# Kernel tuning notes

Hardware: AMD Instinct MI355X
Metric: run time of the kernel (lower is better)

Reference implementation:

```python
import jax, jax.numpy as jnp
import numpy as np

C = 64       # channels; must equal W due to the module's final-Linear-over-W quirk
D = 768      # context_dim (CLIP)
G = 32       # GroupNorm groups
EPS = 1e-5


def setup_inputs() -> dict:
    key = jax.random.key(0)
    ks = jax.random.split(key, 10)
    s = 0.02
    return {
        "x": jax.random.normal(ks[0], (4, C, 64, 64), jnp.float32),
        "context": jax.random.normal(ks[1], (4, 77, D), jnp.float32),
        "gn_scale": jnp.ones((C,), jnp.float32),
        "gn_bias": jnp.zeros((C,), jnp.float32),
        "qkv_w": jax.random.normal(ks[2], (3 * C, C), jnp.float32) * s,  # conv1x1 (out,in)
        "qkv_b": jnp.zeros((3 * C,), jnp.float32),
        "proj_w": jax.random.normal(ks[3], (C, C), jnp.float32) * s,
        "proj_b": jnp.zeros((C,), jnp.float32),
        "ln_scale": jnp.ones((C,), jnp.float32),
        "ln_bias": jnp.zeros((C,), jnp.float32),
        "wq": jax.random.normal(ks[4], (C, C), jnp.float32) * s,   # stored (in,out)
        "bq": jnp.zeros((C,), jnp.float32),
        "wk": jax.random.normal(ks[5], (D, C), jnp.float32) * s,
        "bk": jnp.zeros((C,), jnp.float32),
        "wv": jax.random.normal(ks[6], (D, C), jnp.float32) * s,
        "bv": jnp.zeros((C,), jnp.float32),
        "wo": jax.random.normal(ks[7], (C, C), jnp.float32) * s,
        "bo": jnp.zeros((C,), jnp.float32),
    }


def _group_norm(x, scale, bias):
    B, Ch, H, W = x.shape
    xg = x.reshape(B, G, Ch // G, H, W)
    mu = xg.mean(axis=(2, 3, 4), keepdims=True)
    var = xg.var(axis=(2, 3, 4), keepdims=True)
    xn = ((xg - mu) * jax.lax.rsqrt(var + EPS)).reshape(B, Ch, H, W)
    return xn * scale[None, :, None, None] + bias[None, :, None, None]


def _layer_norm(x, scale, bias):
    mu = x.mean(-1, keepdims=True)
    var = x.var(-1, keepdims=True)
    return (x - mu) * jax.lax.rsqrt(var + EPS) * scale + bias


def reference(x, context, gn_scale, gn_bias, qkv_w, qkv_b, proj_w, proj_b,
              ln_scale, ln_bias, wq, bq, wk, bk, wv, bv, wo, bo):
    B, Ch, H, W = x.shape
    N = H * W
    scale = 1.0 / jnp.sqrt(jnp.asarray(Ch, x.dtype))

    # --- self-attention over spatial positions ---
    h = _group_norm(x, gn_scale, gn_bias)
    qkv = jnp.einsum('bchw,oc->bhwo', h, qkv_w) + qkv_b     # conv 1x1 -> (B,H,W,3C)
    qkv = qkv.reshape(B, N, 3 * Ch)
    q, k, v = jnp.split(qkv, 3, axis=-1)                    # each (B,N,C)
    attn = jax.nn.softmax(jnp.einsum('bnc,bmc->bnm', q, k) * scale, axis=-1)
    self_out = jnp.einsum('bnm,bmc->bnc', attn, v)
    self_out = self_out.transpose(0, 2, 1).reshape(B, Ch, H, W)
    h = x + jnp.einsum('bchw,oc->bohw', self_out, proj_w) + proj_b[None, :, None, None]

    # --- cross-attention with text context ---
    tf = _layer_norm(h.reshape(B, Ch, N).transpose(0, 2, 1), ln_scale, ln_bias)  # (B,N,C)
    tq = tf @ wq + bq                                        # (B,N,C)
    tk = context @ wk + bk                                   # (B,T,C)
    tv = context @ wv + bv                                   # (B,T,C)
    tattn = jax.nn.softmax(jnp.einsum('bnc,btc->bnt', tq, tk) * scale, axis=-1)
    tout = jnp.einsum('bnt,btc->bnc', tattn, tv)             # (B,N,C)
    t4 = tout.transpose(0, 2, 1).reshape(B, Ch, H, W)
    # faithful to source: extra transpose(1,2)+reshape scramble, then Linear over last axis (W==C)
    scr = jnp.transpose(t4, (0, 2, 1, 3)).reshape(B, Ch, H, W)
    h = h + scr @ wo + bo
    return h
```

## Files before the change

kernel.cpp:

```cpp
#include <hip/hip_runtime.h>
#include <cstdint>
#include <cstddef>

#define BN 4
#define CN 64
#define NN 4096
#define GN 32
#define TN 77
#define DN 768
#define EPSV 1e-5f
#define SCALEV 0.125f
#define LOG2E 1.4426950408889634f
#define NSPLIT 8

typedef __bf16 bf16_t;
typedef __attribute__((ext_vector_type(8))) __bf16 bf16x8;
typedef __attribute__((ext_vector_type(4))) __bf16 bf16x4;
typedef __attribute__((ext_vector_type(4))) float f32x4;

#define EXP2(x) __builtin_amdgcn_exp2f(x)

__device__ __forceinline__ f32x4 mfma16(bf16x8 a, bf16x8 b, f32x4 c) {
  return __builtin_amdgcn_mfma_f32_16x16x32_bf16(a, b, c, 0, 0, 0);
}
__device__ __forceinline__ f32x4 zero4() { return (f32x4){0.f, 0.f, 0.f, 0.f}; }

__device__ __forceinline__ void gload16(const void* g, void* l) {
  __builtin_amdgcn_global_load_lds(
      (const __attribute__((address_space(1))) void*)g,
      (__attribute__((address_space(3))) void*)l, 16, 0, 0);
}

__device__ __forceinline__ int fragpos(int o) {
  return ((o >> 2) & 3) * 16 + ((o >> 4) & 1) * 4 + ((o >> 5) & 1) * 8 + (o & 3);
}
__device__ __forceinline__ int vperm(int p) {
  return (p & 32) + ((p >> 2) & 3) * 8 + ((p >> 4) & 1) * 4 + (p & 3);
}
__device__ __forceinline__ int perm96(int t) {
  int u = t & 31;
  return (t & ~31) + (((u & 15) >> 2) << 3) + ((u >> 4) << 2) + (u & 3);
}

__global__ __launch_bounds__(256) void k_pre(const float* __restrict__ x,
    float* __restrict__ gpart,
    const float* __restrict__ ctx,
    const float* __restrict__ wk, const float* __restrict__ bk,
    const float* __restrict__ wv, const float* __restrict__ bv,
    bf16_t* __restrict__ tko, bf16_t* __restrict__ tvo) {
  __shared__ float ss[4], ssq[4];
  __shared__ float cr[768];
  __shared__ float red[4][64];
  int bx = blockIdx.x;
  int tid = threadIdx.x;
  if (bx < 256) {
    const float4* base = reinterpret_cast<const float4*>(x + (size_t)bx * 4096);
    float s = 0.f, sq = 0.f;
    for (int i = tid; i < 1024; i += 256) {
      float4 v = base[i];
      s  += v.x + v.y + v.z + v.w;
      sq += v.x*v.x + v.y*v.y + v.z*v.z + v.w*v.w;
    }
    for (int off = 32; off; off >>= 1) { s += __shfl_down(s, off); sq += __shfl_down(sq, off); }
    int w = tid >> 6, l = tid & 63;
    if (l == 0) { ss[w] = s; ssq[w] = sq; }
    __syncthreads();
    if (tid == 0) {
      gpart[bx * 2]     = ss[0] + ss[1] + ss[2] + ss[3];
      gpart[bx * 2 + 1] = ssq[0] + ssq[1] + ssq[2] + ssq[3];
    }
    return;
  }
  int bt = bx - 256;
  int b = bt / 96, t = bt % 96;
  if (t >= 77) {
    if (tid < 64) {
      if (t < 80) tko[((size_t)(b * 80) + t) * 64 + tid] = (bf16_t)0.f;
      tvo[((size_t)(b * 64) + tid) * 96 + perm96(t)] = (bf16_t)0.f;
    }
    return;
  }
  const float* src = ctx + ((size_t)(b * TN) + t) * 768;
  for (int i = tid; i < 768; i += 256) cr[i] = src[i];
  __syncthreads();
  int o = tid & 63, sec = tid >> 6;
  int sel = sec & 1, dh = sec >> 1;
  const float* w = (sel ? wv : wk) + dh * 384 * 64;
  const float* c0 = cr + dh * 384;
  float acc = 0.f;
  for (int d = 0; d < 384; d++) acc += c0[d] * w[d * 64 + o];
  red[sec][o] = acc;
  __syncthreads();
  if (tid < 128) {
    int s2 = tid >> 6; int oo = tid & 63;
    float r = red[s2][oo] + red[s2 + 2][oo] + (s2 ? bv[oo] : bk[oo]);
    if (s2 == 0)
      tko[((size_t)(b * 80) + t) * 64 + (fragpos(oo) ^ ((t & 7) << 3))] = (bf16_t)r;
    else
      tvo[((size_t)(b * 64) + oo) * 96 + perm96(t)] = (bf16_t)r;
  }
}

__global__ __launch_bounds__(256) void k_gn_qkv(const float* __restrict__ x,
    const float* __restrict__ gpart,
    const float* __restrict__ gns, const float* __restrict__ gnb,
    const float* __restrict__ qkvw, const float* __restrict__ qkvb,
    bf16_t* __restrict__ qb, bf16_t* __restrict__ kb, bf16_t* __restrict__ vT) {
  __shared__ float hn[64][36];
  __shared__ float wqkT[64][129];
  __shared__ float wv2[64][64];
  int bx = blockIdx.x; int b = bx >> 7; int t0 = (bx & 127) << 5;
  int tid = threadIdx.x;
  for (int i = tid; i < 2048; i += 256) {
    float4 v = reinterpret_cast<const float4*>(qkvw)[i];
    int base = i << 2; int o = base >> 6, cc = base & 63;
    wqkT[cc][o] = v.x; wqkT[cc + 1][o] = v.y; wqkT[cc + 2][o] = v.z; wqkT[cc + 3][o] = v.w;
  }
  for (int i = tid; i < 1024; i += 256) {
    float4 v = reinterpret_cast<const float4*>(qkvw + 8192)[i];
    int base = i << 2; int ch = base >> 6, cc = base & 63;
    *reinterpret_cast<float4*>(&wv2[ch][cc]) = v;
  }
  {
    int c = tid >> 2, p0 = (tid & 3) << 3;
    float4 gp = *reinterpret_cast<const float4*>(gpart + (((b << 5) + (c >> 1)) << 2));
    float mu = (gp.x + gp.z) * (1.f / 8192.f);
    float e2 = (gp.y + gp.w) * (1.f / 8192.f);
    float rs = rsqrtf(e2 - mu * mu + EPSV);
    float sc = gns[c] * rs, bi = gnb[c] - mu * sc;
    const float* xp = x + ((size_t)(b * 64 + c)) * NN + t0 + p0;
    float4 v1 = *reinterpret_cast<const float4*>(xp);
    float4 v2 = *reinterpret_cast<const float4*>(xp + 4);
    hn[c][p0+0] = v1.x*sc+bi; hn[c][p0+1] = v1.y*sc+bi;
    hn[c][p0+2] = v1.z*sc+bi; hn[c][p0+3] = v1.w*sc+bi;
    hn[c][p0+4] = v2.x*sc+bi; hn[c][p0+5] = v2.y*sc+bi;
    hn[c][p0+6] = v2.z*sc+bi; hn[c][p0+7] = v2.w*sc+bi;
  }
  __syncthreads();
  {
    int o0 = tid & 63, p0 = (tid >> 6) << 3;
    int pq = fragpos(o0);
    float acc0[8], acc1[8];
    float b0 = qkvb[o0], b1 = qkvb[64 + o0];
    #pragma unroll
    for (int m = 0; m < 8; m++) { acc0[m] = b0; acc1[m] = b1; }
    for (int cc = 0; cc < 64; ++cc) {
      float4 h0 = *reinterpret_cast<const float4*>(&hn[cc][p0]);
      float4 h1 = *reinterpret_cast<const float4*>(&hn[cc][p0 + 4]);
      float w0 = wqkT[cc][o0];
      float w1 = wqkT[cc][64 + o0];
      acc0[0] += h0.x*w0; acc0[1] += h0.y*w0; acc0[2] += h0.z*w0; acc0[3] += h0.w*w0;
      acc0[4] += h1.x*w0; acc0[5] += h1.y*w0; acc0[6] += h1.z*w0; acc0[7] += h1.w*w0;
      acc1[0] += h0.x*w1; acc1[1] += h0.y*w1; acc1[2] += h0.z*w1; acc1[3] += h0.w*w1;
      acc1[4] += h1.x*w1; acc1[5] += h1.y*w1; acc1[6] += h1.z*w1; acc1[7] += h1.w*w1;
    }
    size_t rowbase = ((size_t)(b * NN) + t0 + p0) << 6;
    #pragma unroll
    for (int j = 0; j < 8; j++) {
      qb[rowbase + ((size_t)j << 6) + pq] = (bf16_t)(acc0[j] * (SCALEV * LOG2E));
      kb[rowbase + ((size_t)j << 6) + (pq ^ (j << 3))] = (bf16_t)acc1[j];
    }
  }
  {
    int p2 = tid & 31, ob = tid >> 5;
    int kk = t0 + p2;
    int colsw = vperm(kk & 63) ^ (ob << 3);
    float acc[8];
    #pragma unroll
    for (int m = 0; m < 8; m++) acc[m] = qkvb[128 + ob + 8*m];
    for (int c0 = 0; c0 < 64; c0 += 4) {
      float h0 = hn[c0][p2], h1 = hn[c0+1][p2], h2 = hn[c0+2][p2], h3 = hn[c0+3][p2];
      #pragma unroll
      for (int m = 0; m < 8; m++) {
        float4 w4 = *reinterpret_cast<const float4*>(&wv2[ob + 8*m][c0]);
        acc[m] += h0*w4.x + h1*w4.y + h2*w4.z + h3*w4.w;
      }
    }
    size_t vbase = ((size_t)(b * 64)) * NN + (size_t)(kk & ~63) + colsw;
    #pragma unroll
    for (int m = 0; m < 8; m++)
      vT[vbase + (size_t)(ob + 8*m) * NN] = (bf16_t)acc[m];
  }
}

__global__ __launch_bounds__(256, 4) void k_attn(const bf16_t* __restrict__ qb,
    const bf16_t* __restrict__ kb, const bf16_t* __restrict__ vT,
    bf16_t* __restrict__ opart, float* __restrict__ mpart, float* __restrict__ lpart) {
  __shared__ __align__(16) bf16_t smem[2][8192];
  int bx = blockIdx.x;
  int xcd = bx & 7;
  int b = xcd >> 1;
  int inner = ((bx >> 3) << 1) | (xcd & 1);
  int split = inner >> 5;
  int qblk = inner & 31;
  int tid = threadIdx.x; int w = tid >> 6, l = tid & 63;
  int lo = l & 15, g = l >> 4;
  int qbase = (qblk << 7) + (w << 5);
  const bf16_t* qrowA = qb + (((size_t)(b * NN) + qbase + lo) << 6) + g * 16;
  const bf16_t* qrowB = qrowA + (16 << 6);
  bf16x8 qfA0 = *reinterpret_cast<const bf16x8*>(qrowA);
  bf16x8 qfA1 = *reinterpret_cast<const bf16x8*>(qrowA + 8);
  bf16x8 qfB0 = *reinterpret_cast<const bf16x8*>(qrowB);
  bf16x8 qfB1 = *reinterpret_cast<const bf16x8*>(qrowB + 8);
  f32x4 oaccA[4], oaccB[4];
  #pragma unroll
  for (int nt = 0; nt < 4; nt++) {
    oaccA[nt] = zero4();
    oaccB[nt] = zero4();
  }
  float mA = -8.f, lA = 0.f, mB = -8.f, lB = 0.f;
  const bf16_t* kbB = kb + ((size_t)b * NN << 6);
  const bf16_t* vB  = vT + ((size_t)b * 64) * NN;
  int kt0 = split << 9;

  int off0 = tid * 8;
  int off1 = 2048 + tid * 8;
  int ch0 = off0 >> 6, sl0 = off0 & 63;
  int ch1 = off1 >> 6, sl1 = off1 & 63;

  {
    const bf16_t* kT = kbB + ((size_t)kt0 << 6);
    gload16(kT + off0, &smem[0][off0]);
    gload16(kT + off1, &smem[0][off1]);
    gload16(vB + (size_t)ch0 * NN + kt0 + sl0, &smem[0][4096 + off0]);
    gload16(vB + (size_t)ch1 * NN + kt0 + sl1, &smem[0][4096 + off1]);
  }
  __syncthreads();

  #pragma unroll 1
  for (int t = 0; t < 8; ++t) {
    int cur = t & 1;
    if (t < 7) {
      int kn = kt0 + ((t + 1) << 6);
      const bf16_t* kT = kbB + ((size_t)kn << 6);
      gload16(kT + off0, &smem[cur ^ 1][off0]);
      gload16(kT + off1, &smem[cur ^ 1][off1]);
      gload16(vB + (size_t)ch0 * NN + kn + sl0, &smem[cur ^ 1][4096 + off0]);
      gload16(vB + (size_t)ch1 * NN + kn + sl1, &smem[cur ^ 1][4096 + off1]);
    }
    const bf16_t* sK = smem[cur];
    const bf16_t* sV = smem[cur] + 4096;
    f32x4 sA[4], sB[4];
    #pragma unroll
    for (int c = 0; c < 4; c++) {
      int kk = (c << 4) + lo;
      int o1 = (g << 4) ^ ((kk & 7) << 3);
      bf16x8 kf0 = *reinterpret_cast<const bf16x8*>(sK + (kk << 6) + o1);
      bf16x8 kf1 = *reinterpret_cast<const bf16x8*>(sK + (kk << 6) + (o1 ^ 8));
      sA[c] = mfma16(kf0, qfA0, zero4());
      sA[c] = mfma16(kf1, qfA1, sA[c]);
      sB[c] = mfma16(kf0, qfB0, zero4());
      sB[c] = mfma16(kf1, qfB1, sB[c]);
    }
    float pmaxA = -1e30f, pmaxB = -1e30f;
    #pragma unroll
    for (int c = 0; c < 4; c++)
      #pragma unroll
      for (int r = 0; r < 4; r++) {
        pmaxA = fmaxf(pmaxA, sA[c][r]);
        pmaxB = fmaxf(pmaxB, sB[c][r]);
      }
    if (!__all(pmaxA - mA <= 8.f)) {
      pmaxA = fmaxf(pmaxA, __shfl_xor(pmaxA, 16));
      pmaxA = fmaxf(pmaxA, __shfl_xor(pmaxA, 32));
      float mn = fmaxf(mA, pmaxA);
      float corr = EXP2(mA - mn);
      lA *= corr; mA = mn;
      float fr[4];
      #pragma unroll
      for (int r = 0; r < 4; r++) fr[r] = __shfl(corr, (g << 2) + r);
      #pragma unroll
      for (int nt = 0; nt < 4; nt++)
        #pragma unroll
        for (int r = 0; r < 4; r++) oaccA[nt][r] *= fr[r];
    }
    if (!__all(pmaxB - mB <= 8.f)) {
      pmaxB = fmaxf(pmaxB, __shfl_xor(pmaxB, 16));
      pmaxB = fmaxf(pmaxB, __shfl_xor(pmaxB, 32));
      float mn = fmaxf(mB, pmaxB);
      float corr = EXP2(mB - mn);
      lB *= corr; mB = mn;
      float fr[4];
      #pragma unroll
      for (int r = 0; r < 4; r++) fr[r] = __shfl(corr, (g << 2) + r);
      #pragma unroll
      for (int nt = 0; nt < 4; nt++)
        #pragma unroll
        for (int r = 0; r < 4; r++) oaccB[nt][r] *= fr[r];
    }
    bf16x8 vf[4];
    #pragma unroll
    for (int nt = 0; nt < 4; nt++) {
      int ch = lo + (nt << 4);
      vf[nt] = *reinterpret_cast<const bf16x8*>(sV + (ch << 6) + ((g ^ (ch & 7)) << 3));
    }
    float lsA0 = 0.f, lsA1 = 0.f, lsB0 = 0.f, lsB1 = 0.f;
    #pragma unroll
    for (int c = 0; c < 4; c++)
      #pragma unroll
      for (int r = 0; r < 4; r++) {
        float pa = EXP2(sA[c][r] - mA);
        float pb = EXP2(sB[c][r] - mB);
        sA[c][r] = pa; sB[c][r] = pb;
        if (c & 1) { lsA1 += pa; lsB1 += pb; } else { lsA0 += pa; lsB0 += pb; }
      }
    lA += lsA0 + lsA1;
    lB += lsB0 + lsB1;
    bf16x8 paA0, paA1, paB0, paB1;
    #pragma unroll
    for (int i = 0; i < 8; i++) {
      paA0[i] = (bf16_t)sA[i >> 2][i & 3]; paA1[i] = (bf16_t)sA[2 + (i >> 2)][i & 3];
      paB0[i] = (bf16_t)sB[i >> 2][i & 3]; paB1[i] = (bf16_t)sB[2 + (i >> 2)][i & 3];
    }
    #pragma unroll
    for (int nt = 0; nt < 4; ++nt) {
      oaccA[nt] = mfma16(paA0, vf[nt], oaccA[nt]);
      oaccB[nt] = mfma16(paB0, vf[nt], oaccB[nt]);
    }
    #pragma unroll
    for (int nt = 0; nt < 4; nt++) {
      int ch = lo + (nt << 4);
      vf[nt] = *reinterpret_cast<const bf16x8*>(sV + (ch << 6) + (((4 + g) ^ (ch & 7)) << 3));
    }
    #pragma unroll
    for (int nt = 0; nt < 4; ++nt) {
      oaccA[nt] = mfma16(paA1, vf[nt], oaccA[nt]);
      oaccB[nt] = mfma16(paB1, vf[nt], oaccB[nt]);
    }
    __syncthreads();
  }

  lA += __shfl_xor(lA, 16); lA += __shfl_xor(lA, 32);
  lB += __shfl_xor(lB, 16); lB += __shfl_xor(lB, 32);

  size_t ob = ((size_t)(split * BN + b)) * NN + qbase;
  float liA[4], liB[4];
  #pragma unroll
  for (int r = 0; r < 4; r++) {
    liA[r] = 1.0f / __shfl(lA, (g << 2) + r);
    liB[r] = 1.0f / __shfl(lB, (g << 2) + r);
  }
  #pragma unroll
  for (int nt = 0; nt < 4; nt++)
    #pragma unroll
    for (int r = 0; r < 4; r++) {
      opart[((ob + (g << 2) + r) << 6) + lo + (nt << 4)] = (bf16_t)(oaccA[nt][r] * liA[r]);
      opart[((ob + 16 + (g << 2) + r) << 6) + lo + (nt << 4)] = (bf16_t)(oaccB[nt][r] * liB[r]);
    }
  if (l < 16) { mpart[ob + l] = mA; lpart[ob + l] = lA; }
  else if (l < 32) { mpart[ob + 16 + lo] = mB; lpart[ob + 16 + lo] = lB; }
}

__global__ __launch_bounds__(256) void k_proj_ln_tq(const float* __restrict__ x,
    const bf16_t* __restrict__ opart, const float* __restrict__ mpart, const float* __restrict__ lpart,
    const float* __restrict__ projw, const float* __restrict__ projb,
    const float* __restrict__ lns, const float* __restrict__ lnb,
    const float* __restrict__ wq, const float* __restrict__ bq,
    float* __restrict__ h2, bf16_t* __restrict__ tq) {
  __shared__ float wcomb[16][NSPLIT];
  __shared__ float sob[16][65];
  __shared__ float h2l[64][17];
  __shared__ float r1[16][16], r2[16][16];
  __shared__ float mu_s[16], rs_s[16];
  int bx = blockIdx.x; int b = bx >> 8; int t0 = (bx & 255) << 4;
  int tid = threadIdx.x;
  if (tid < 16) {
    int p = tid, q = t0 + p;
    float ms[NSPLIT];
    float mstar = -1e30f;
    #pragma unroll
    for (int s = 0; s < NSPLIT; s++) {
      ms[s] = mpart[((size_t)(s * BN + b)) * NN + q];
      mstar = fmaxf(mstar, ms[s]);
    }
    float co[NSPLIT]; float denom = 0.f;
    #pragma unroll
    for (int s = 0; s < NSPLIT; s++) {
      co[s] = EXP2(ms[s] - mstar) * lpart[((size_t)(s * BN + b)) * NN + q];
      denom += co[s];
    }
    float inv = 1.0f / denom;
    #pragma unroll
    for (int s = 0; s < NSPLIT; s++) wcomb[p][s] = co[s] * inv;
  }
  __syncthreads();
  {
    int p = tid >> 4, c0 = (tid & 15) << 2;
    int q = t0 + p;
    float acc[4] = {0.f, 0.f, 0.f, 0.f};
    #pragma unroll
    for (int s = 0; s < NSPLIT; s++) {
      bf16x4 v = *reinterpret_cast<const bf16x4*>(
          opart + ((((size_t)(s * BN + b)) * NN + q) << 6) + c0);
      float wv = wcomb[p][s];
      #pragma unroll
      for (int j = 0; j < 4; j++) acc[j] += wv * (float)v[j];
    }
    #pragma unroll
    for (int j = 0; j < 4; j++) sob[p][c0 + j] = acc[j];
  }
  __syncthreads();
  {
    int p = tid & 15, ob = tid >> 4;
    float acc[4];
    #pragma unroll
    for (int m = 0; m < 4; m++) {
      int o = ob + 16*m;
      acc[m] = projb[o] + x[((size_t)(b * 64) + o) * NN + t0 + p];
    }
    for (int cc = 0; cc < 64; ++cc) {
      float sv = sob[p][cc];
      #pragma unroll
      for (int m = 0; m < 4; m++) acc[m] += sv * projw[(ob + 16*m) * 64 + cc];
    }
    #pragma unroll
    for (int m = 0; m < 4; m++) {
      int o = ob + 16*m;
      h2[((size_t)(b * 64) + o) * NN + t0 + p] = acc[m];
      h2l[o][p] = acc[m];
    }
  }
  __syncthreads();
  {
    int p = tid & 15, og = tid >> 4;
    float s = 0.f, sq = 0.f;
    #pragma unroll
    for (int j = 0; j < 4; j++) { float v = h2l[og * 4 + j][p]; s += v; sq += v*v; }
    r1[og][p] = s; r2[og][p] = sq;
  }
  __syncthreads();
  if (tid < 16) {
    float s = 0.f, sq = 0.f;
    #pragma unroll
    for (int j = 0; j < 16; j++) { s += r1[j][tid]; sq += r2[j][tid]; }
    float mu = s * (1.f/64.f);
    float var = sq * (1.f/64.f) - mu*mu;
    mu_s[tid] = mu; rs_s[tid] = rsqrtf(var + EPSV);
  }
  __syncthreads();
  {
    int p = tid & 15, cb = tid >> 4;
    float mu = mu_s[p], rs = rs_s[p];
    #pragma unroll
    for (int m = 0; m < 4; m++) {
      int c = cb + 16*m;
      sob[p][c] = (h2l[c][p] - mu) * rs * lns[c] + lnb[c];
    }
  }
  __syncthreads();
  {
    int o = tid & 63, pb = tid >> 6;
    int pq = fragpos(o);
    float acc[4];
    #pragma unroll
    for (int m = 0; m < 4; m++) acc[m] = bq[o];
    for (int cc = 0; cc < 64; ++cc) {
      float wv = wq[cc * 64 + o];
      #pragma unroll
      for (int m = 0; m < 4; m++) acc[m] += sob[pb + 4*m][cc] * wv;
    }
    #pragma unroll
    for (int m = 0; m < 4; m++) {
      int p = pb + 4*m;
      tq[(((size_t)(b * NN) + t0 + p) << 6) + pq] = (bf16_t)(acc[m] * (SCALEV * LOG2E));
    }
  }
}

__global__ __launch_bounds__(256) void k_crossf(const bf16_t* __restrict__ tq,
    const bf16_t* __restrict__ tk, const bf16_t* __restrict__ tv,
    const float* __restrict__ wo, const float* __restrict__ bo,
    const float* __restrict__ h2, float* __restrict__ out) {
  __shared__ __align__(16) bf16_t tkl[80][64];
  __shared__ __align__(16) bf16_t tvl[64][104];
  __shared__ __align__(16) bf16_t woT[64][64];
  __shared__ __align__(16) bf16_t toutT[64][64];
  int bx = blockIdx.x; int b = bx >> 6; int c1 = bx & 63;
  int tid = threadIdx.x; int wv_ = tid >> 6; int l = tid & 63;
  int lo = l & 15, g = l >> 4;
  {
    const uint4* src = reinterpret_cast<const uint4*>(tk + (size_t)b * 80 * 64);
    uint4* dst = reinterpret_cast<uint4*>(&tkl[0][0]);
    for (int i = tid; i < 640; i += 256) dst[i] = src[i];
  }
  {
    const uint4* src = reinterpret_cast<const uint4*>(tv + (size_t)b * 64 * 96);
    uint4* dst = reinterpret_cast<uint4*>(&tvl[0][0]);
    for (int i = tid; i < 768; i += 256) {
      int row = i / 12, j = i % 12;
      dst[row * 13 + j] = src[i];
    }
  }
  for (int i = tid; i < 4096; i += 256) {
    int k = i >> 6, w = i & 63;
    int vp = vperm(k);
    woT[w][(((vp >> 3) ^ (w & 7)) << 3) + (vp & 7)] = (bf16_t)wo[i];
  }
  __syncthreads();
  int n0 = (c1 << 6) + (wv_ << 4);
  const bf16_t* qrow = tq + (((size_t)(b * NN) + n0 + lo) << 6) + g * 16;
  bf16x8 qf0 = *reinterpret_cast<const bf16x8*>(qrow);
  bf16x8 qf1 = *reinterpret_cast<const bf16x8*>(qrow + 8);
  f32x4 sa[5];
  #pragma unroll
  for (int ti = 0; ti < 5; ti++) {
    int tok = ti * 16 + lo;
    int o1 = (g << 4) ^ ((tok & 7) << 3);
    bf16x8 kf0 = *reinterpret_cast<const bf16x8*>(&tkl[tok][0] + o1);
    bf16x8 kf1 = *reinterpret_cast<const bf16x8*>(&tkl[tok][0] + (o1 ^ 8));
    f32x4 z = mfma16(kf0, qf0, zero4());
    sa[ti] = mfma16(kf1, qf1, z);
  }
  float p[5][4];
  float mx = -1e30f;
  #pragma unroll
  for (int ti = 0; ti < 5; ti++)
    #pragma unroll
    for (int r = 0; r < 4; r++)
      if (ti * 16 + (g << 2) + r < TN) mx = fmaxf(mx, sa[ti][r]);
  mx = fmaxf(mx, __shfl_xor(mx, 16));
  mx = fmaxf(mx, __shfl_xor(mx, 32));
  float ls = 0.f;
  #pragma unroll
  for (int ti = 0; ti < 5; ti++)
    #pragma unroll
    for (int r = 0; r < 4; r++) {
      float pv = (ti * 16 + (g << 2) + r < TN) ? EXP2(sa[ti][r] - mx) : 0.f;
      p[ti][r] = pv; ls += pv;
    }
  ls += __shfl_xor(ls, 16); ls += __shfl_xor(ls, 32);
  float linv = 1.0f / ls;
  bf16x8 pa[3];
  #pragma unroll
  for (int c = 0; c < 3; c++)
    #pragma unroll
    for (int i = 0; i < 8; i++)
      pa[c][i] = (bf16_t)p[2 * c + (i >> 2)][i & 3];
  f32x4 oacc[4];
  #pragma unroll
  for (int nt = 0; nt < 4; nt++) oacc[nt] = zero4();
  #pragma unroll
  for (int c = 0; c < 3; c++)
    #pragma unroll
    for (int nt = 0; nt < 4; nt++) {
      bf16x8 vf = *reinterpret_cast<const bf16x8*>(&tvl[nt * 16 + lo][0] + c * 32 + g * 8);
      oacc[nt] = mfma16(pa[c], vf, oacc[nt]);
    }
  float li[4];
  #pragma unroll
  for (int r = 0; r < 4; r++) li[r] = __shfl(linv, (g << 2) + r);
  int hh = wv_ & 1, cp = wv_ >> 1;
  #pragma unroll
  for (int nt = 0; nt < 4; nt++) {
    int ch = nt * 16 + lo;
    int basegroup = cp * 4 + g;
    int col = ((basegroup ^ (ch & 7)) << 3) + hh * 4;
    bf16_t tmp[4];
    #pragma unroll
    for (int r = 0; r < 4; r++) tmp[r] = (bf16_t)(oacc[nt][r] * li[r]);
    *reinterpret_cast<uint2*>(&toutT[ch][col]) = *reinterpret_cast<const uint2*>(tmp);
  }
  __syncthreads();
  f32x4 o2[4];
  #pragma unroll
  for (int wt = 0; wt < 4; wt++) o2[wt] = zero4();
  #pragma unroll
  for (int f = 0; f < 2; f++) {
    int c2r = wv_ * 16 + lo;
    int agrp = ((f * 4 + g) ^ (c2r & 7)) << 3;
    bf16x8 af = *reinterpret_cast<const bf16x8*>(&toutT[c2r][agrp]);
    #pragma unroll
    for (int wt = 0; wt < 4; wt++) {
      int wrow = wt * 16 + lo;
      int bgrp = ((f * 4 + g) ^ (wrow & 7)) << 3;
      bf16x8 bf_ = *reinterpret_cast<const bf16x8*>(&woT[wrow][bgrp]);
      o2[wt] = mfma16(af, bf_, o2[wt]);
    }
  }
  const float* h2r = h2 + ((size_t)(b * 64) + c1) * NN;
  float* outr = out + ((size_t)(b * 64) + c1) * NN;
  float bov[4];
  #pragma unroll
  for (int wt = 0; wt < 4; wt++) bov[wt] = bo[wt * 16 + lo];
  #pragma unroll
  for (int wt = 0; wt < 4; wt++)
    #pragma unroll
    for (int r = 0; r < 4; r++) {
      int c2 = wv_ * 16 + (g << 2) + r;
      int pos = (c2 << 6) + wt * 16 + lo;
      outr[pos] = o2[wt][r] + h2r[pos] + bov[wt];
    }
}

extern "C" void kernel_launch(void* const* d_in, const int* in_sizes, int n_in,
                              void* d_out, int out_size, void* d_ws, size_t ws_size,
                              hipStream_t stream) {
  const float* x     = (const float*)d_in[0];
  const float* ctx   = (const float*)d_in[1];
  const float* gns   = (const float*)d_in[2];
  const float* gnb   = (const float*)d_in[3];
  const float* qkvw  = (const float*)d_in[4];
  const float* qkvb  = (const float*)d_in[5];
  const float* projw = (const float*)d_in[6];
  const float* projb = (const float*)d_in[7];
  const float* lns   = (const float*)d_in[8];
  const float* lnb   = (const float*)d_in[9];
  const float* wq    = (const float*)d_in[10];
  const float* bq    = (const float*)d_in[11];
  const float* wk    = (const float*)d_in[12];
  const float* bk    = (const float*)d_in[13];
  const float* wv    = (const float*)d_in[14];
  const float* bv    = (const float*)d_in[15];
  const float* wo    = (const float*)d_in[16];
  const float* bo    = (const float*)d_in[17];
  float* out = (float*)d_out;

  char* ws = (char*)d_ws;
  float* gpart = (float*)ws;
  bf16_t* qb   = (bf16_t*)(ws + 4096);
  bf16_t* kbuf = qb + (size_t)BN * NN * 64;
  bf16_t* vT   = kbuf + (size_t)BN * NN * 64;
  bf16_t* opart = vT + (size_t)BN * NN * 64;
  float* mpart = (float*)(opart + (size_t)NSPLIT * BN * NN * 64);
  float* lpart = mpart + (size_t)NSPLIT * BN * NN;
  float* h2    = lpart + (size_t)NSPLIT * BN * NN;
  bf16_t* tkb16 = (bf16_t*)(h2 + (size_t)BN * NN * 64);
  bf16_t* tvb16 = tkb16 + (size_t)BN * 80 * 64;
  bf16_t* tqb16 = qb;

  k_pre<<<dim3(256 + BN * 96), dim3(256), 0, stream>>>(x, gpart, ctx, wk, bk, wv, bv,
                                                       tkb16, tvb16);
  k_gn_qkv<<<dim3(512), dim3(256), 0, stream>>>(x, gpart, gns, gnb, qkvw, qkvb,
                                                qb, kbuf, vT);
  k_attn<<<dim3(1024), dim3(256), 0, stream>>>(qb, kbuf, vT, opart, mpart, lpart);
  k_proj_ln_tq<<<dim3(1024), dim3(256), 0, stream>>>(x, opart, mpart, lpart, projw, projb,
                                                     lns, lnb, wq, bq, h2, tqb16);
  k_crossf<<<dim3(256), dim3(256), 0, stream>>>(tqb16, tkb16, tvb16, wo, bo, h2, out);
}
```

Before: 76.22 us.

## Process 64 query rows per wave in self-attention to double K/V reuse

Each wave in the attention kernel now handles four 16-row query fragments instead of two. This halves the number of blocks and doubles how much work each K/V tile staged in shared memory feeds into the MFMAs, cutting LDS and global traffic per query. The lazy-rescale skip based on a wave vote is dropped, so the max correction now always runs. Register pressure rises, the occupancy hint is relaxed, and with fewer blocks latency hiding may be weaker.

```diff
diff --git a/kernel.cpp b/kernel.cpp
--- a/kernel.cpp
+++ b/kernel.cpp
@@ -183,7 +183,7 @@
   }
 }
 
-__global__ __launch_bounds__(256, 4) void k_attn(const bf16_t* __restrict__ qb,
+__global__ __launch_bounds__(256) void k_attn(const bf16_t* __restrict__ qb,
     const bf16_t* __restrict__ kb, const bf16_t* __restrict__ vT,
     bf16_t* __restrict__ opart, float* __restrict__ mpart, float* __restrict__ lpart) {
   __shared__ __align__(16) bf16_t smem[2][8192];
@@ -191,24 +191,25 @@
   int xcd = bx & 7;
   int b = xcd >> 1;
   int inner = ((bx >> 3) << 1) | (xcd & 1);
-  int split = inner >> 5;
-  int qblk = inner & 31;
+  int split = inner >> 4;
+  int qblk = inner & 15;
   int tid = threadIdx.x; int w = tid >> 6, l = tid & 63;
   int lo = l & 15, g = l >> 4;
-  int qbase = (qblk << 7) + (w << 5);
-  const bf16_t* qrowA = qb + (((size_t)(b * NN) + qbase + lo) << 6) + g * 16;
-  const bf16_t* qrowB = qrowA + (16 << 6);
-  bf16x8 qfA0 = *reinterpret_cast<const bf16x8*>(qrowA);
-  bf16x8 qfA1 = *reinterpret_cast<const bf16x8*>(qrowA + 8);
-  bf16x8 qfB0 = *reinterpret_cast<const bf16x8*>(qrowB);
-  bf16x8 qfB1 = *reinterpret_cast<const bf16x8*>(qrowB + 8);
-  f32x4 oaccA[4], oaccB[4];
-  #pragma unroll
-  for (int nt = 0; nt < 4; nt++) {
-    oaccA[nt] = zero4();
-    oaccB[nt] = zero4();
-  }
-  float mA = -8.f, lA = 0.f, mB = -8.f, lB = 0.f;
+  int qbase = (qblk << 8) + (w << 6);
+  bf16x8 qf[4][2];
+  #pragma unroll
+  for (int F = 0; F < 4; F++) {
+    const bf16_t* qrow = qb + (((size_t)(b * NN) + qbase + F * 16 + lo) << 6) + g * 16;
+    qf[F][0] = *reinterpret_cast<const bf16x8*>(qrow);
+    qf[F][1] = *reinterpret_cast<const bf16x8*>(qrow + 8);
+  }
+  f32x4 oacc[4][4];
+  #pragma unroll
+  for (int F = 0; F < 4; F++)
+    #pragma unroll
+    for (int nt = 0; nt < 4; nt++) oacc[F][nt] = zero4();
+  float m_[4] = {-8.f, -8.f, -8.f, -8.f};
+  float l_[4] = {0.f, 0.f, 0.f, 0.f};
   const bf16_t* kbB = kb + ((size_t)b * NN << 6);
   const bf16_t* vB  = vT + ((size_t)b * 64) * NN;
   int kt0 = split << 9;
@@ -240,53 +241,38 @@
     }
     const bf16_t* sK = smem[cur];
     const bf16_t* sV = smem[cur] + 4096;
-    f32x4 sA[4], sB[4];
+    f32x4 s[4][4];
     #pragma unroll
     for (int c = 0; c < 4; c++) {
       int kk = (c << 4) + lo;
       int o1 = (g << 4) ^ ((kk & 7) << 3);
       bf16x8 kf0 = *reinterpret_cast<const bf16x8*>(sK + (kk << 6) + o1);
       bf16x8 kf1 = *reinterpret_cast<const bf16x8*>(sK + (kk << 6) + (o1 ^ 8));
-      sA[c] = mfma16(kf0, qfA0, zero4());
-      sA[c] = mfma16(kf1, qfA1, sA[c]);
-      sB[c] = mfma16(kf0, qfB0, zero4());
-      sB[c] = mfma16(kf1, qfB1, sB[c]);
-    }
-    float pmaxA = -1e30f, pmaxB = -1e30f;
-    #pragma unroll
-    for (int c = 0; c < 4; c++)
-      #pragma unroll
-      for (int r = 0; r < 4; r++) {
-        pmaxA = fmaxf(pmaxA, sA[c][r]);
-        pmaxB = fmaxf(pmaxB, sB[c][r]);
+      #pragma unroll
+      for (int F = 0; F < 4; F++) {
+        s[F][c] = mfma16(kf0, qf[F][0], zero4());
+        s[F][c] = mfma16(kf1, qf[F][1], s[F][c]);
       }
-    if (!__all(pmaxA - mA <= 8.f)) {
-      pmaxA = fmaxf(pmaxA, __shfl_xor(pmaxA, 16));
-      pmaxA = fmaxf(pmaxA, __shfl_xor(pmaxA, 32));
-      float mn = fmaxf(mA, pmaxA);
-      float corr = EXP2(mA - mn);
-      lA *= corr; mA = mn;
+    }
+    #pragma unroll
+    for (int F = 0; F < 4; F++) {
+      float pmax = -1e30f;
+      #pragma unroll
+      for (int c = 0; c < 4; c++)
+        #pragma unroll
+        for (int r = 0; r < 4; r++) pmax = fmaxf(pmax, s[F][c][r]);
+      pmax = fmaxf(pmax, __shfl_xor(pmax, 16));
+      pmax = fmaxf(pmax, __shfl_xor(pmax, 32));
+      float mn = fmaxf(m_[F], pmax);
+      float corr = EXP2(m_[F] - mn);
+      l_[F] *= corr; m_[F] = mn;
       float fr[4];
       #pragma unroll
       for (int r = 0; r < 4; r++) fr[r] = __shfl(corr, (g << 2) + r);
       #pragma unroll
       for (int nt = 0; nt < 4; nt++)
         #pragma unroll
-        for (int r = 0; r < 4; r++) oaccA[nt][r] *= fr[r];
-    }
-    if (!__all(pmaxB - mB <= 8.f)) {
-      pmaxB = fmaxf(pmaxB, __shfl_xor(pmaxB, 16));
-      pmaxB = fmaxf(pmaxB, __shfl_xor(pmaxB, 32));
-      float mn = fmaxf(mB, pmaxB);
-      float corr = EXP2(mB - mn);
-      lB *= corr; mB = mn;
-      float fr[4];
-      #pragma unroll
-      for (int r = 0; r < 4; r++) fr[r] = __shfl(corr, (g << 2) + r);
-      #pragma unroll
-      for (int nt = 0; nt < 4; nt++)
-        #pragma unroll
-        for (int r = 0; r < 4; r++) oaccB[nt][r] *= fr[r];
+        for (int r = 0; r < 4; r++) oacc[F][nt][r] *= fr[r];
     }
     bf16x8 vf[4];
     #pragma unroll
@@ -294,61 +280,68 @@
       int ch = lo + (nt << 4);
       vf[nt] = *reinterpret_cast<const bf16x8*>(sV + (ch << 6) + ((g ^ (ch & 7)) << 3));
     }
-    float lsA0 = 0.f, lsA1 = 0.f, lsB0 = 0.f, lsB1 = 0.f;
-    #pragma unroll
-    for (int c = 0; c < 4; c++)
-      #pragma unroll
-      for (int r = 0; r < 4; r++) {
-        float pa = EXP2(sA[c][r] - mA);
-        float pb = EXP2(sB[c][r] - mB);
-        sA[c][r] = pa; sB[c][r] = pb;
-        if (c & 1) { lsA1 += pa; lsB1 += pb; } else { lsA0 += pa; lsB0 += pb; }
+    #pragma unroll
+    for (int F = 0; F < 4; F++) {
+      float ls0 = 0.f, ls1 = 0.f;
+      #pragma unroll
+      for (int c = 0; c < 4; c++)
+        #pragma unroll
+        for (int r = 0; r < 4; r++) {
+          float pv = EXP2(s[F][c][r] - m_[F]);
+          s[F][c][r] = pv;
+          if (c & 1) ls1 += pv; else ls0 += pv;
+        }
+      l_[F] += ls0 + ls1;
+    }
+    bf16x8 pa[4][2];
+    #pragma unroll
+    for (int F = 0; F < 4; F++)
+      #pragma unroll
+      for (int i = 0; i < 8; i++) {
+        pa[F][0][i] = (bf16_t)s[F][i >> 2][i & 3];
+        pa[F][1][i] = (bf16_t)s[F][2 + (i >> 2)][i & 3];
       }
-    lA += lsA0 + lsA1;
-    lB += lsB0 + lsB1;
-    bf16x8 paA0, paA1, paB0, paB1;
-    #pragma unroll
-    for (int i = 0; i < 8; i++) {
-      paA0[i] = (bf16_t)sA[i >> 2][i & 3]; paA1[i] = (bf16_t)sA[2 + (i >> 2)][i & 3];
-      paB0[i] = (bf16_t)sB[i >> 2][i & 3]; paB1[i] = (bf16_t)sB[2 + (i >> 2)][i & 3];
-    }
-    #pragma unroll
-    for (int nt = 0; nt < 4; ++nt) {
-      oaccA[nt] = mfma16(paA0, vf[nt], oaccA[nt]);
-      oaccB[nt] = mfma16(paB0, vf[nt], oaccB[nt]);
-    }
+    #pragma unroll
+    for (int nt = 0; nt < 4; ++nt)
+      #pragma unroll
+      for (int F = 0; F < 4; F++)
+        oacc[F][nt] = mfma16(pa[F][0], vf[nt], oacc[F][nt]);
     #pragma unroll
     for (int nt = 0; nt < 4; nt++) {
       int ch = lo + (nt << 4);
       vf[nt] = *reinterpret_cast<const bf16x8*>(sV + (ch << 6) + (((4 + g) ^ (ch & 7)) << 3));
     }
     #pragma unroll
-    for (int nt = 0; nt < 4; ++nt) {
-      oaccA[nt] = mfma16(paA1, vf[nt], oaccA[nt]);
-      oaccB[nt] = mfma16(paB1, vf[nt], oaccB[nt]);
-    }
+    for (int nt = 0; nt < 4; ++nt)
+      #pragma unroll
+      for (int F = 0; F < 4; F++)
+        oacc[F][nt] = mfma16(pa[F][1], vf[nt], oacc[F][nt]);
     __syncthreads();
   }
 
-  lA += __shfl_xor(lA, 16); lA += __shfl_xor(lA, 32);
-  lB += __shfl_xor(lB, 16); lB += __shfl_xor(lB, 32);
+  #pragma unroll
+  for (int F = 0; F < 4; F++) {
+    l_[F] += __shfl_xor(l_[F], 16);
+    l_[F] += __shfl_xor(l_[F], 32);
+  }
 
   size_t ob = ((size_t)(split * BN + b)) * NN + qbase;
-  float liA[4], liB[4];
-  #pragma unroll
-  for (int r = 0; r < 4; r++) {
-    liA[r] = 1.0f / __shfl(lA, (g << 2) + r);
-    liB[r] = 1.0f / __shfl(lB, (g << 2) + r);
-  }
-  #pragma unroll
-  for (int nt = 0; nt < 4; nt++)
-    #pragma unroll
-    for (int r = 0; r < 4; r++) {
-      opart[((ob + (g << 2) + r) << 6) + lo + (nt << 4)] = (bf16_t)(oaccA[nt][r] * liA[r]);
-      opart[((ob + 16 + (g << 2) + r) << 6) + lo + (nt << 4)] = (bf16_t)(oaccB[nt][r] * liB[r]);
-    }
-  if (l < 16) { mpart[ob + l] = mA; lpart[ob + l] = lA; }
-  else if (l < 32) { mpart[ob + 16 + lo] = mB; lpart[ob + 16 + lo] = lB; }
+  #pragma unroll
+  for (int F = 0; F < 4; F++) {
+    float li[4];
+    #pragma unroll
+    for (int r = 0; r < 4; r++) li[r] = 1.0f / __shfl(l_[F], (g << 2) + r);
+    #pragma unroll
+    for (int nt = 0; nt < 4; nt++)
+      #pragma unroll
+      for (int r = 0; r < 4; r++)
+        opart[((ob + F * 16 + (g << 2) + r) << 6) + lo + (nt << 4)] =
+            (bf16_t)(oacc[F][nt][r] * li[r]);
+  }
+  if (l < 16)      { mpart[ob + lo] = m_[0];      lpart[ob + lo] = l_[0]; }
+  else if (l < 32) { mpart[ob + 16 + lo] = m_[1]; lpart[ob + 16 + lo] = l_[1]; }
+  else if (l < 48) { mpart[ob + 32 + lo] = m_[2]; lpart[ob + 32 + lo] = l_[2]; }
+  else             { mpart[ob + 48 + lo] = m_[3]; lpart[ob + 48 + lo] = l_[3]; }
 }
 
 __global__ __launch_bounds__(256) void k_proj_ln_tq(const float* __restrict__ x,
@@ -632,7 +625,7 @@
                                                        tkb16, tvb16);
   k_gn_qkv<<<dim3(512), dim3(256), 0, stream>>>(x, gpart, gns, gnb, qkvw, qkvb,
                                                 qb, kbuf, vT);
-  k_attn<<<dim3(1024), dim3(256), 0, stream>>>(qb, kbuf, vT, opart, mpart, lpart);
+  k_attn<<<dim3(512), dim3(256), 0, stream>>>(qb, kbuf, vT, opart, mpart, lpart);
   k_proj_ln_tq<<<dim3(1024), dim3(256), 0, stream>>>(x, opart, mpart, lpart, projw, projb,
                                                      lns, lnb, wq, bq, h2, tqb16);
   k_crossf<<<dim3(256), dim3(256), 0, stream>>>(tqb16, tkb16, tvb16, wo, bo, h2, out);
```

Measured after the change: 92.12 us. +20.9%, slower.
